# Performance work log

Hardware: AMD Instinct MI355X
Metric: run time of the kernel (lower is better)

## Reference

```python
import jax, jax.numpy as jnp
import numpy as np

N_NODES = 100000
N_EDGES = 1250000
IN_DIM = 64
OUT_DIM = 64
N_BASES = 16
L2_EPS = 1e-12  # torch F.normalize eps


def setup_inputs() -> dict:
    key = jax.random.key(0)
    ks = jax.random.split(key, 7)
    return {
        "x": jax.random.normal(ks[0], (N_NODES, IN_DIM), dtype=jnp.float32),
        "edge_index": jax.random.randint(ks[1], (2, N_EDGES), 0, N_NODES, dtype=jnp.int64)
        if jax.config.jax_enable_x64 else jax.random.randint(ks[1], (2, N_EDGES), 0, N_NODES, dtype=jnp.int32),
        "basis_msg_wt": jax.random.normal(ks[2], (IN_DIM, OUT_DIM, N_BASES), dtype=jnp.float32) * 0.1,
        "basis_msg_bias": jax.random.normal(ks[3], (OUT_DIM, N_BASES), dtype=jnp.float32) * 0.1,
        "basis_self_wt": jax.random.normal(ks[4], (IN_DIM, OUT_DIM, N_BASES), dtype=jnp.float32) * 0.1,
        "basis_self_bias": jax.random.normal(ks[5], (OUT_DIM, N_BASES), dtype=jnp.float32) * 0.1,
        "lin_comb": jax.random.normal(ks[6], (1, N_BASES), dtype=jnp.float32) * 0.1,
    }


def reference(x, edge_index, basis_msg_wt, basis_msg_bias, basis_self_wt, basis_self_bias, lin_comb):
    c = lin_comb[0]  # [B]
    # Reconstruct relation-specific weights from bases on the fly.
    W_msg = jnp.einsum('iob,b->io', basis_msg_wt, c)      # [in, out]
    b_msg = basis_msg_bias @ c                             # [out]
    W_self = jnp.einsum('iob,b->io', basis_self_wt, c)    # [in, out]
    b_self = basis_self_bias @ c                           # [out]

    src, dst = edge_index[0], edge_index[1]
    # gather x_j, per-relation linear message
    msg = x[src] @ W_msg + b_msg                           # [E, out]
    # scatter-add aggregate to destination nodes
    agg = jax.ops.segment_sum(msg, dst, num_segments=x.shape[0])  # [N, out]
    # self transform (skip_linear=True path)
    x_self = x @ W_self + b_self                           # [N, out]
    out = agg + x_self
    # F.normalize(p=2, dim=-1): divide by max(norm, eps)
    norm = jnp.linalg.norm(out, axis=-1, keepdims=True)
    return out / jnp.maximum(norm, L2_EPS)
```

## Files before the change

### kernel.cpp

```cpp
#include <hip/hip_runtime.h>

constexpr int NN = 100000;
constexpr int NE = 1250000;
constexpr int D  = 64;
constexpr int NB = 16;

constexpr int NC = 196;
constexpr int PA_BLOCKS = 512;
constexpr int NCB = NC * PA_BLOCKS;
constexpr int NSBLK = (NCB + 255) / 256;
constexpr int EPB = (NE + PA_BLOCKS - 1) / PA_BLOCKS;

typedef __attribute__((ext_vector_type(8))) short short8v;
typedef __attribute__((ext_vector_type(4))) float float4v;

__device__ __forceinline__ unsigned short f2bf(float f) {
    unsigned u = __float_as_uint(f);
    u += 0x7fffu + ((u >> 16) & 1u);
    return (unsigned short)(u >> 16);
}
__device__ __forceinline__ float bf2f(unsigned short h) {
    return __uint_as_float(((unsigned)h) << 16);
}

constexpr int PRE_COMBINE = 8192 + 128;
constexpr int PRE_TOTAL   = PRE_COMBINE + NN * (D / 4);
constexpr int PREP_GRID   = PA_BLOCKS + (PRE_TOTAL + 255) / 256;

__global__ void prep_kernel(const float* __restrict__ wm,
                            const float* __restrict__ bm,
                            const float* __restrict__ wsf,
                            const float* __restrict__ bsf,
                            const float* __restrict__ lc,
                            const float* __restrict__ x,
                            const int* __restrict__ ei,
                            int* __restrict__ bhist,
                            unsigned short* __restrict__ wct,
                            float* __restrict__ B,
                            unsigned short* __restrict__ xb)
{
    __shared__ int h[NC];
    const int tid = threadIdx.x;

    if (blockIdx.x < PA_BLOCKS) {
        if (tid < NC) h[tid] = 0;
        __syncthreads();
        const int begin = blockIdx.x * EPB;
        const int end = min(NE, begin + EPB);
        for (int e = begin + tid; e < end; e += 256)
            atomicAdd(&h[ei[NE + e] >> 9], 1);
        __syncthreads();
        if (tid < NC) bhist[tid * PA_BLOCKS + blockIdx.x] = h[tid];
        return;
    }

    int t = (blockIdx.x - PA_BLOCKS) * 256 + tid;
    if (t < PRE_COMBINE) {
        float c[NB];
        #pragma unroll
        for (int b = 0; b < NB; ++b) c[b] = lc[b];
        const float* p;
        if (t < 4096)      p = wm  + t * NB;
        else if (t < 8192) p = wsf + (t - 4096) * NB;
        else if (t < 8256) p = bm  + (t - 8192) * NB;
        else               p = bsf + (t - 8256) * NB;
        float s = 0.f;
        #pragma unroll
        for (int b = 0; b < NB; ++b) s += p[b] * c[b];

        if (t < 4096) {
            int i = t >> 6, o = t & 63;
            wct[o * 128 + i] = f2bf(s);
        } else if (t < 8192) {
            int u = t - 4096;
            int i = u >> 6, o = u & 63;
            wct[o * 128 + 64 + i] = f2bf(s);
        } else if (t < 8256) {
            B[t - 8192] = s;
        } else {
            B[64 + (t - 8256)] = s;
        }
    } else if (t < PRE_TOTAL) {
        int k = t - PRE_COMBINE;
        float4 v = reinterpret_cast<const float4*>(x)[k];
        ushort4 o;
        o.x = f2bf(v.x); o.y = f2bf(v.y); o.z = f2bf(v.z); o.w = f2bf(v.w);
        reinterpret_cast<ushort4*>(xb)[k] = o;
    }
}

__global__ void scan_block(int* __restrict__ data,
                           int* __restrict__ partials, int n)
{
    __shared__ int tmp[256];
    int tid = threadIdx.x;
    int i = blockIdx.x * 256 + tid;
    int c = (i < n) ? data[i] : 0;
    int v = c;
    tmp[tid] = v;
    __syncthreads();
    for (int d = 1; d < 256; d <<= 1) {
        int t = (tid >= d) ? tmp[tid - d] : 0;
        __syncthreads();
        v += t;
        tmp[tid] = v;
        __syncthreads();
    }
    if (i < n) data[i] = v - c;
    if (tid == 255) partials[blockIdx.x] = v;
}

__global__ void add_offsets(int* __restrict__ data,
                            const int* __restrict__ partials, int n)
{
    __shared__ int red[256];
    const int tid = threadIdx.x;
    int s = 0;
    for (int i = tid; i < blockIdx.x; i += 256) s += partials[i];
    red[tid] = s;
    __syncthreads();
    for (int d = 128; d; d >>= 1) {
        if (tid < d) red[tid] += red[tid + d];
        __syncthreads();
    }
    int i = blockIdx.x * 256 + tid;
    if (i < n) data[i] += red[0];
}

__global__ __launch_bounds__(256)
void passA_scatter(const int* __restrict__ ei,
                   const int* __restrict__ starts,
                   int* __restrict__ pair_buf)
{
    __shared__ int cnt[NC];
    __shared__ int base[NC];
    const int tid = threadIdx.x;
    for (int j = tid; j < NC; j += 256) {
        cnt[j] = 0;
        base[j] = starts[j * PA_BLOCKS + blockIdx.x];
    }
    __syncthreads();

    const int begin = blockIdx.x * EPB;
    const int end = min(NE, begin + EPB);
    for (int e = begin + tid; e < end; e += 256) {
        int src = ei[e];
        int dst = ei[NE + e];
        int key = dst >> 9;
        int pos = base[key] + atomicAdd(&cnt[key], 1);
        pair_buf[pos] = (src << 9) | (dst & 511);
    }
}

__global__ __launch_bounds__(512)
void passB_sort(const int* __restrict__ pair_buf,
                const int* __restrict__ starts,
                int* __restrict__ sorted_src,
                int* __restrict__ node_start,
                int* __restrict__ counts)
{
    __shared__ int tmp[512];
    __shared__ int cur[512];
    const int b = blockIdx.x;
    const int s = starts[b * PA_BLOCKS];
    const int e = (b == NC - 1) ? NE : starts[(b + 1) * PA_BLOCKS];
    const int tid = threadIdx.x;

    tmp[tid] = 0;
    __syncthreads();
    for (int i = s + tid; i < e; i += 512)
        atomicAdd(&tmp[pair_buf[i] & 511], 1);
    __syncthreads();

    int c0 = tmp[tid];
    int v = c0;
    __syncthreads();
    tmp[tid] = v;
    __syncthreads();
    for (int d = 1; d < 512; d <<= 1) {
        int t = (tid >= d) ? tmp[tid - d] : 0;
        __syncthreads();
        v += t;
        tmp[tid] = v;
        __syncthreads();
    }
    int excl = v - c0;

    const int n = (b << 9) + tid;
    if (n < NN) {
        counts[n] = c0;
        node_start[n] = s + excl;
    }
    cur[tid] = excl;
    __syncthreads();

    for (int i = s + tid; i < e; i += 512) {
        int w = pair_buf[i];
        int pos = atomicAdd(&cur[w & 511], 1);
        sorted_src[s + pos] = w >> 9;
    }
}

__global__ __launch_bounds__(256)
void gather_kernel(const unsigned int* __restrict__ xbd,
                   const int* __restrict__ sorted_src,
                   const int* __restrict__ node_start,
                   const int* __restrict__ counts,
                   float* __restrict__ agg)
{
    const int wave = threadIdx.x >> 6;
    const int lane = threadIdx.x & 63;
    const int half = lane >> 5;
    const int dq   = lane & 31;
    const int n = blockIdx.x * 4 + wave;

    const int deg = counts[n];
    const int j0 = node_start[n];

    int idxv = 0;
    if (lane < deg) idxv = sorted_src[j0 + lane];

    float aL[8], aH[8];
    #pragma unroll
    for (int p = 0; p < 8; ++p) { aL[p] = 0.f; aH[p] = 0.f; }

    const int dmain = min(deg, 64);
    for (int jj = 0; jj < dmain; jj += 16) {
        #pragma unroll
        for (int p = 0; p < 8; ++p) {
            int pos = jj + 2 * p + half;
            int srcl = __builtin_amdgcn_ds_bpermute(pos << 2, idxv);
            unsigned int u = xbd[(((unsigned)srcl) << 5) | (unsigned)dq];
            u = (pos < dmain) ? u : 0u;
            aL[p] += __uint_as_float(u << 16);
            aH[p] += __uint_as_float(u & 0xffff0000u);
        }
    }
    for (int pos = 64 + half; pos < deg; pos += 2) {
        int srcl = sorted_src[j0 + pos];
        unsigned int u = xbd[(((unsigned)srcl) << 5) | (unsigned)dq];
        aL[0] += __uint_as_float(u << 16);
        aH[0] += __uint_as_float(u & 0xffff0000u);
    }

    float sL = ((aL[0] + aL[1]) + (aL[2] + aL[3])) + ((aL[4] + aL[5]) + (aL[6] + aL[7]));
    float sH = ((aH[0] + aH[1]) + (aH[2] + aH[3])) + ((aH[4] + aH[5]) + (aH[6] + aH[7]));

    sL += __shfl_xor(sL, 32, 64);
    sH += __shfl_xor(sH, 32, 64);

    if (half == 0) {
        float2 v = make_float2(sL, sH);
        *reinterpret_cast<float2*>(agg + (size_t)n * D + 2 * dq) = v;
    }
}

constexpr int NTILES = NN / 16;
constexpr int TBLOCKS = 640;

__global__ __launch_bounds__(256)
void transform_mfma(float* __restrict__ out,
                    const unsigned short* __restrict__ xb,
                    const unsigned short* __restrict__ wct,
                    const float* __restrict__ B,
                    const int* __restrict__ counts)
{
    const int lane = threadIdx.x & 63;
    const int gq = lane >> 4;
    const int c  = lane & 15;
    const int wglob = blockIdx.x * 4 + (threadIdx.x >> 6);

    short8v wf[4][4];
    #pragma unroll
    for (int t = 0; t < 4; ++t)
        #pragma unroll
        for (int ks = 0; ks < 4; ++ks) {
            int o = t * 16 + c;
            int k0 = ks * 32 + gq * 8;
            wf[t][ks] = *reinterpret_cast<const short8v*>(wct + o * 128 + k0);
        }
    float bmv[4], bsv[4];
    #pragma unroll
    for (int t = 0; t < 4; ++t) {
        bmv[t] = B[t * 16 + c];
        bsv[t] = B[64 + t * 16 + c];
    }

    for (int tile = wglob; tile < NTILES; tile += TBLOCKS * 4) {
        const int n0 = tile * 16;
        const size_t arow = (size_t)(n0 + c) * D;

        float4v acc[4];
        #pragma unroll
        for (int t = 0; t < 4; ++t) acc[t] = (float4v){0.f, 0.f, 0.f, 0.f};

        #pragma unroll
        for (int ks = 0; ks < 2; ++ks) {
            const float* p = out + arow + ks * 32 + gq * 8;
            float4v f0 = *reinterpret_cast<const float4v*>(p);
            float4v f1 = *reinterpret_cast<const float4v*>(p + 4);
            short8v a;
            a[0] = (short)f2bf(f0[0]); a[1] = (short)f2bf(f0[1]);
            a[2] = (short)f2bf(f0[2]); a[3] = (short)f2bf(f0[3]);
            a[4] = (short)f2bf(f1[0]); a[5] = (short)f2bf(f1[1]);
            a[6] = (short)f2bf(f1[2]); a[7] = (short)f2bf(f1[3]);
            #pragma unroll
            for (int t = 0; t < 4; ++t)
                acc[t] = __builtin_amdgcn_mfma_f32_16x16x32_bf16(a, wf[t][ks], acc[t], 0, 0, 0);
        }
        #pragma unroll
        for (int ks = 2; ks < 4; ++ks) {
            short8v a = *reinterpret_cast<const short8v*>(xb + arow + (ks - 2) * 32 + gq * 8);
            #pragma unroll
            for (int t = 0; t < 4; ++t)
                acc[t] = __builtin_amdgcn_mfma_f32_16x16x32_bf16(a, wf[t][ks], acc[t], 0, 0, 0);
        }

        float dg[4];
        #pragma unroll
        for (int q = 0; q < 4; ++q) dg[q] = (float)counts[n0 + gq * 4 + q];

        float ss[4] = {0.f, 0.f, 0.f, 0.f};
        #pragma unroll
        for (int t = 0; t < 4; ++t)
            #pragma unroll
            for (int q = 0; q < 4; ++q) {
                float v = acc[t][q] + dg[q] * bmv[t] + bsv[t];
                acc[t][q] = v;
                ss[q] += v * v;
            }
        #pragma unroll
        for (int off = 1; off <= 8; off <<= 1)
            #pragma unroll
            for (int q = 0; q < 4; ++q) ss[q] += __shfl_xor(ss[q], off, 64);

        float sc[4];
        #pragma unroll
        for (int q = 0; q < 4; ++q) sc[q] = 1.f / fmaxf(sqrtf(ss[q]), 1e-12f);

        #pragma unroll
        for (int t = 0; t < 4; ++t)
            #pragma unroll
            for (int q = 0; q < 4; ++q)
                out[(size_t)(n0 + gq * 4 + q) * D + t * 16 + c] = acc[t][q] * sc[q];
    }
}

extern "C" void kernel_launch(void* const* d_in, const int* in_sizes, int n_in,
                              void* d_out, int out_size, void* d_ws, size_t ws_size,
                              hipStream_t stream)
{
    const float* x   = (const float*)d_in[0];
    const int*   ei  = (const int*)d_in[1];
    const float* wm  = (const float*)d_in[2];
    const float* bm  = (const float*)d_in[3];
    const float* wsf = (const float*)d_in[4];
    const float* bsf = (const float*)d_in[5];
    const float* lc  = (const float*)d_in[6];

    float* out = (float*)d_out;

    float* Bv         = (float*)d_ws;
    unsigned short* wct = (unsigned short*)(Bv + 128);
    int* starts       = (int*)(wct + 8192);
    int* partials     = starts + NCB;
    int* counts       = partials + 512;
    int* node_start   = counts + NN;
    int* pair_buf     = node_start + NN;
    int* sorted_src   = pair_buf + NE;
    unsigned short* xb = (unsigned short*)(sorted_src + NE);

    prep_kernel<<<PREP_GRID, 256, 0, stream>>>(
        wm, bm, wsf, bsf, lc, x, ei, starts, wct, Bv, xb);

    scan_block<<<NSBLK, 256, 0, stream>>>(starts, partials, NCB);
    add_offsets<<<NSBLK, 256, 0, stream>>>(starts, partials, NCB);

    passA_scatter<<<PA_BLOCKS, 256, 0, stream>>>(ei, starts, pair_buf);

    passB_sort<<<NC, 512, 0, stream>>>(pair_buf, starts,
                                       sorted_src, node_start, counts);

    gather_kernel<<<NN / 4, 256, 0, stream>>>(
        (const unsigned int*)xb, sorted_src, node_start, counts, out);

    transform_mfma<<<TBLOCKS, 256, 0, stream>>>(out, xb, wct, Bv, counts);
}
```

Measured before the change: 86.89 us.

## Fuse neighbor gather with MFMA transform and L2 normalize in one kernel

Merges the gather kernel and the MFMA transform kernel. Each block now aggregates 16 destination nodes into bf16 rows in shared memory, appends their own bf16 features, and multiplies the tile by the combined weights with MFMA. The row L2 norm is reduced across waves through shared memory. This removes the fp32 round trip of the aggregate through global memory and one kernel launch, at the cost of more serialized work per block and extra barriers.

```diff
diff --git a/kernel.cpp b/kernel.cpp
--- a/kernel.cpp
+++ b/kernel.cpp
@@ -18,9 +18,6 @@
     unsigned u = __float_as_uint(f);
     u += 0x7fffu + ((u >> 16) & 1u);
     return (unsigned short)(u >> 16);
-}
-__device__ __forceinline__ float bf2f(unsigned short h) {
-    return __uint_as_float(((unsigned)h) << 16);
 }
 
 constexpr int PRE_COMBINE = 8192 + 128;
@@ -202,147 +199,114 @@
 }
 
 __global__ __launch_bounds__(256)
-void gather_kernel(const unsigned int* __restrict__ xbd,
-                   const int* __restrict__ sorted_src,
-                   const int* __restrict__ node_start,
-                   const int* __restrict__ counts,
-                   float* __restrict__ agg)
-{
+void gather_mfma(const unsigned int* __restrict__ xbd,
+                 const int* __restrict__ sorted_src,
+                 const int* __restrict__ node_start,
+                 const int* __restrict__ counts,
+                 const unsigned short* __restrict__ wct,
+                 const float* __restrict__ B,
+                 float* __restrict__ out)
+{
+    __shared__ unsigned aA[16][68];
+    __shared__ float ssp[4][16];
+    __shared__ int degs[16];
+
     const int wave = threadIdx.x >> 6;
     const int lane = threadIdx.x & 63;
     const int half = lane >> 5;
     const int dq   = lane & 31;
-    const int n = blockIdx.x * 4 + wave;
-
-    const int deg = counts[n];
-    const int j0 = node_start[n];
-
-    int idxv = 0;
-    if (lane < deg) idxv = sorted_src[j0 + lane];
-
-    float aL[8], aH[8];
-    #pragma unroll
-    for (int p = 0; p < 8; ++p) { aL[p] = 0.f; aH[p] = 0.f; }
-
-    const int dmain = min(deg, 64);
-    for (int jj = 0; jj < dmain; jj += 16) {
-        #pragma unroll
-        for (int p = 0; p < 8; ++p) {
-            int pos = jj + 2 * p + half;
-            int srcl = __builtin_amdgcn_ds_bpermute(pos << 2, idxv);
+    const int n0 = blockIdx.x * 16;
+
+    const int c  = lane & 15;
+    const int gq = lane >> 4;
+    const int t  = wave;
+
+    short8v wf[4];
+    #pragma unroll
+    for (int ks = 0; ks < 4; ++ks)
+        wf[ks] = *reinterpret_cast<const short8v*>(wct + (t * 16 + c) * 128 + ks * 32 + gq * 8);
+    const float bmv = B[t * 16 + c];
+    const float bsv = B[64 + t * 16 + c];
+
+    #pragma unroll
+    for (int k = 0; k < 4; ++k) {
+        const int row = (wave << 2) + k;
+        const int n = n0 + row;
+        const int deg = counts[n];
+        const int j0 = node_start[n];
+
+        int idxv = 0;
+        if (lane < deg) idxv = sorted_src[j0 + lane];
+
+        float aL[8], aH[8];
+        #pragma unroll
+        for (int p = 0; p < 8; ++p) { aL[p] = 0.f; aH[p] = 0.f; }
+
+        const int dmain = min(deg, 64);
+        for (int jj = 0; jj < dmain; jj += 16) {
+            #pragma unroll
+            for (int p = 0; p < 8; ++p) {
+                int pos = jj + 2 * p + half;
+                int srcl = __builtin_amdgcn_ds_bpermute(pos << 2, idxv);
+                unsigned int u = xbd[(((unsigned)srcl) << 5) | (unsigned)dq];
+                u = (pos < dmain) ? u : 0u;
+                aL[p] += __uint_as_float(u << 16);
+                aH[p] += __uint_as_float(u & 0xffff0000u);
+            }
+        }
+        for (int pos = 64 + half; pos < deg; pos += 2) {
+            int srcl = sorted_src[j0 + pos];
             unsigned int u = xbd[(((unsigned)srcl) << 5) | (unsigned)dq];
-            u = (pos < dmain) ? u : 0u;
-            aL[p] += __uint_as_float(u << 16);
-            aH[p] += __uint_as_float(u & 0xffff0000u);
+            aL[0] += __uint_as_float(u << 16);
+            aH[0] += __uint_as_float(u & 0xffff0000u);
         }
-    }
-    for (int pos = 64 + half; pos < deg; pos += 2) {
-        int srcl = sorted_src[j0 + pos];
-        unsigned int u = xbd[(((unsigned)srcl) << 5) | (unsigned)dq];
-        aL[0] += __uint_as_float(u << 16);
-        aH[0] += __uint_as_float(u & 0xffff0000u);
-    }
-
-    float sL = ((aL[0] + aL[1]) + (aL[2] + aL[3])) + ((aL[4] + aL[5]) + (aL[6] + aL[7]));
-    float sH = ((aH[0] + aH[1]) + (aH[2] + aH[3])) + ((aH[4] + aH[5]) + (aH[6] + aH[7]));
-
-    sL += __shfl_xor(sL, 32, 64);
-    sH += __shfl_xor(sH, 32, 64);
-
-    if (half == 0) {
-        float2 v = make_float2(sL, sH);
-        *reinterpret_cast<float2*>(agg + (size_t)n * D + 2 * dq) = v;
-    }
-}
-
-constexpr int NTILES = NN / 16;
-constexpr int TBLOCKS = 640;
-
-__global__ __launch_bounds__(256)
-void transform_mfma(float* __restrict__ out,
-                    const unsigned short* __restrict__ xb,
-                    const unsigned short* __restrict__ wct,
-                    const float* __restrict__ B,
-                    const int* __restrict__ counts)
-{
-    const int lane = threadIdx.x & 63;
-    const int gq = lane >> 4;
-    const int c  = lane & 15;
-    const int wglob = blockIdx.x * 4 + (threadIdx.x >> 6);
-
-    short8v wf[4][4];
-    #pragma unroll
-    for (int t = 0; t < 4; ++t)
-        #pragma unroll
-        for (int ks = 0; ks < 4; ++ks) {
-            int o = t * 16 + c;
-            int k0 = ks * 32 + gq * 8;
-            wf[t][ks] = *reinterpret_cast<const short8v*>(wct + o * 128 + k0);
+
+        float sL = ((aL[0] + aL[1]) + (aL[2] + aL[3])) + ((aL[4] + aL[5]) + (aL[6] + aL[7]));
+        float sH = ((aH[0] + aH[1]) + (aH[2] + aH[3])) + ((aH[4] + aH[5]) + (aH[6] + aH[7]));
+        sL += __shfl_xor(sL, 32, 64);
+        sH += __shfl_xor(sH, 32, 64);
+
+        if (half == 0) {
+            unsigned pk = ((unsigned)f2bf(sH) << 16) | (unsigned)f2bf(sL);
+            aA[row][dq] = pk;
+            if (dq == 0) degs[row] = deg;
+        } else {
+            aA[row][32 + dq] = xbd[(((unsigned)n) << 5) | (unsigned)dq];
         }
-    float bmv[4], bsv[4];
-    #pragma unroll
-    for (int t = 0; t < 4; ++t) {
-        bmv[t] = B[t * 16 + c];
-        bsv[t] = B[64 + t * 16 + c];
-    }
-
-    for (int tile = wglob; tile < NTILES; tile += TBLOCKS * 4) {
-        const int n0 = tile * 16;
-        const size_t arow = (size_t)(n0 + c) * D;
-
-        float4v acc[4];
-        #pragma unroll
-        for (int t = 0; t < 4; ++t) acc[t] = (float4v){0.f, 0.f, 0.f, 0.f};
-
-        #pragma unroll
-        for (int ks = 0; ks < 2; ++ks) {
-            const float* p = out + arow + ks * 32 + gq * 8;
-            float4v f0 = *reinterpret_cast<const float4v*>(p);
-            float4v f1 = *reinterpret_cast<const float4v*>(p + 4);
-            short8v a;
-            a[0] = (short)f2bf(f0[0]); a[1] = (short)f2bf(f0[1]);
-            a[2] = (short)f2bf(f0[2]); a[3] = (short)f2bf(f0[3]);
-            a[4] = (short)f2bf(f1[0]); a[5] = (short)f2bf(f1[1]);
-            a[6] = (short)f2bf(f1[2]); a[7] = (short)f2bf(f1[3]);
-            #pragma unroll
-            for (int t = 0; t < 4; ++t)
-                acc[t] = __builtin_amdgcn_mfma_f32_16x16x32_bf16(a, wf[t][ks], acc[t], 0, 0, 0);
-        }
-        #pragma unroll
-        for (int ks = 2; ks < 4; ++ks) {
-            short8v a = *reinterpret_cast<const short8v*>(xb + arow + (ks - 2) * 32 + gq * 8);
-            #pragma unroll
-            for (int t = 0; t < 4; ++t)
-                acc[t] = __builtin_amdgcn_mfma_f32_16x16x32_bf16(a, wf[t][ks], acc[t], 0, 0, 0);
-        }
-
-        float dg[4];
-        #pragma unroll
-        for (int q = 0; q < 4; ++q) dg[q] = (float)counts[n0 + gq * 4 + q];
-
-        float ss[4] = {0.f, 0.f, 0.f, 0.f};
-        #pragma unroll
-        for (int t = 0; t < 4; ++t)
-            #pragma unroll
-            for (int q = 0; q < 4; ++q) {
-                float v = acc[t][q] + dg[q] * bmv[t] + bsv[t];
-                acc[t][q] = v;
-                ss[q] += v * v;
-            }
-        #pragma unroll
-        for (int off = 1; off <= 8; off <<= 1)
-            #pragma unroll
-            for (int q = 0; q < 4; ++q) ss[q] += __shfl_xor(ss[q], off, 64);
-
-        float sc[4];
-        #pragma unroll
-        for (int q = 0; q < 4; ++q) sc[q] = 1.f / fmaxf(sqrtf(ss[q]), 1e-12f);
-
-        #pragma unroll
-        for (int t = 0; t < 4; ++t)
-            #pragma unroll
-            for (int q = 0; q < 4; ++q)
-                out[(size_t)(n0 + gq * 4 + q) * D + t * 16 + c] = acc[t][q] * sc[q];
+    }
+    __syncthreads();
+
+    float4v acc = (float4v){0.f, 0.f, 0.f, 0.f};
+    #pragma unroll
+    for (int ks = 0; ks < 4; ++ks) {
+        short8v a = *reinterpret_cast<const short8v*>(&aA[c][ks * 16 + gq * 4]);
+        acc = __builtin_amdgcn_mfma_f32_16x16x32_bf16(a, wf[ks], acc, 0, 0, 0);
+    }
+
+    float ss[4];
+    #pragma unroll
+    for (int q = 0; q < 4; ++q) {
+        float dgq = (float)degs[gq * 4 + q];
+        float vv = acc[q] + dgq * bmv + bsv;
+        acc[q] = vv;
+        ss[q] = vv * vv;
+    }
+    #pragma unroll
+    for (int off = 1; off <= 8; off <<= 1)
+        #pragma unroll
+        for (int q = 0; q < 4; ++q) ss[q] += __shfl_xor(ss[q], off, 64);
+    if (c == 0) {
+        #pragma unroll
+        for (int q = 0; q < 4; ++q) ssp[t][gq * 4 + q] = ss[q];
+    }
+    __syncthreads();
+
+    #pragma unroll
+    for (int q = 0; q < 4; ++q) {
+        int row = gq * 4 + q;
+        float tot = (ssp[0][row] + ssp[1][row]) + (ssp[2][row] + ssp[3][row]);
+        float sc = 1.f / fmaxf(sqrtf(tot), 1e-12f);
+        out[(size_t)(n0 + row) * D + t * 16 + c] = acc[q] * sc;
     }
 }
 
@@ -381,8 +345,6 @@
     passB_sort<<<NC, 512, 0, stream>>>(pair_buf, starts,
                                        sorted_src, node_start, counts);
 
-    gather_kernel<<<NN / 4, 256, 0, stream>>>(
-        (const unsigned int*)xb, sorted_src, node_start, counts, out);
-
-    transform_mfma<<<TBLOCKS, 256, 0, stream>>>(out, xb, wct, Bv, counts);
-}
+    gather_mfma<<<NN / 16, 256, 0, stream>>>(
+        (const unsigned int*)xb, sorted_src, node_start, counts, wct, Bv, out);
+}
```

Result: slower. 93.89 us (+8.1%).
